# Optimization experiments

Hardware: AMD Instinct MI355X
Metric: run time of the kernel (lower is better)

The kernel has to match this reference:

```python
import jax
import jax.numpy as jnp
import numpy as np
from jax import lax

DELTA = float(np.exp(-2.0))  # rule-creation density threshold


def codebook_lamb(x):
    """Online growing RBF prototype codebook (ALMMo-style) for one layer.

    x: [N, M]. Returns lamb: [N] normalized density of each sample at its
    assigned rule. Faithful (corrected) semantics of Layer.__call__:
      - SEN = squared L2 norm per sample (over feature dim)
      - global mean / mean squared norm over the batch
      - sequential per-sample: if max RBF density over existing rules < exp(-2),
        append a new rule (prototype=c=x, SENc=||x||^2, support=1);
        else update rule_star. Note the source's `support[rule_star] = +1`
        assigns 1, so the running mean update degenerates to c[rule_star]=x,
        SENc[rule_star]=||x||^2 -- replicated here.
      - distances use the (never-updated) prototypes; bandwidth stau uses c.
    """
    N, M = x.shape
    SENx = jnp.sum(x * x, axis=-1)                      # [N]
    gmean = jnp.mean(x, axis=0)                         # [M]
    base = jnp.mean(SENx) - jnp.sum(gmean * gmean)      # SENgmean - SEN(gmean)
    R = N                                               # worst case: one rule/sample

    protos0 = jnp.zeros((R, M), x.dtype)
    pn20 = jnp.zeros((R,), x.dtype)                     # ||proto_r||^2 (carried)
    c0 = jnp.zeros((R, M), x.dtype)
    cn20 = jnp.zeros((R,), x.dtype)                     # ||c_r||^2 (carried)
    SENc0 = jnp.zeros((R,), x.dtype)
    count0 = jnp.int32(0)

    ridx = jnp.arange(R)

    def step(carry, inp):
        protos, pn2, c, cn2, SENc, count = carry
        xi, sxi = inp                                   # [M], scalar
        valid = ridx < count
        stau = (base + SENc - cn2) * 0.5                # [R]
        dist = sxi + pn2 - 2.0 * (protos @ xi)          # [R] ||xi - proto_r||^2
        dens = jnp.where(valid, jnp.exp(-dist / stau), -jnp.inf)
        idx = jnp.argmax(dens)
        vmax = dens[idx]
        new = (count == 0) | (vmax < DELTA)
        slot = jnp.where(new, count, idx)
        # both branches set c/SENc at slot to xi/sxi (support resets to 1)
        c = c.at[slot].set(xi)
        cn2 = cn2.at[slot].set(sxi)
        SENc = SENc.at[slot].set(sxi)
        # only a new rule writes a prototype (OOB scatter when count==R is dropped)
        protos = protos.at[count].set(jnp.where(new, xi, protos[count]))
        pn2 = pn2.at[count].set(jnp.where(new, sxi, pn2[count]))
        count = count + new.astype(count.dtype)
        return (protos, pn2, c, cn2, SENc, count), slot

    (protos, pn2, c, cn2, SENc, count), rules = lax.scan(
        step, (protos0, pn20, c0, cn20, SENc0, count0), (x, SENx)
    )

    # final densities of all samples under all (valid) rules: [R, N]
    stau = (base + SENc - cn2) * 0.5                    # [R]
    dist = SENx[None, :] + pn2[:, None] - 2.0 * (protos @ x.T)
    dens = jnp.where((ridx < count)[:, None], jnp.exp(-dist / stau[:, None]), 0.0)
    dens_xn = dens[rules, jnp.arange(N)]                # density at assigned rule
    lamb = dens_xn / jnp.sum(dens, axis=0)              # normalize over rules
    return lamb


def setup_inputs() -> dict:
    key = jax.random.key(0)
    k = jax.random.split(key, 5)
    N, D_IN, D_H, D_OUT = 2048, 2048, 2048, 1024
    s0 = 1.0 / np.sqrt(D_IN)
    s1 = 1.0 / np.sqrt(D_H)
    return {
        "x": jax.random.normal(k[0], (N, D_IN), jnp.float32),
        "W0": jax.random.normal(k[1], (D_H, D_IN), jnp.float32) * s0,
        "b0": jax.random.normal(k[2], (D_H,), jnp.float32) * s0,
        "W1": jax.random.normal(k[3], (D_OUT, D_H), jnp.float32) * s1,
        "b1": jax.random.normal(k[4], (D_OUT,), jnp.float32) * s1,
    }


def reference(x, W0, b0, W1, b1):
    lambs = []
    h = x
    for W, b in ((W0, b0), (W1, b1)):
        lambs.append(codebook_lamb(h))          # per-layer codebook on layer input
        h = jax.nn.sigmoid(h @ W.T + b)         # torch.nn.Linear + sigmoid
    return h, jnp.stack(lambs)                  # ([N, d_out], [n_layers, N])
```

## Files before the change

### kernel.cpp

```cpp
#include <hip/hip_runtime.h>
#include <cstdint>
#include <cstddef>


#define DELTA_F 0.13533528323661270f
#define MBYTE (1u << 20)

typedef __bf16 bf16;
typedef bf16 bf16x8 __attribute__((ext_vector_type(8)));
typedef bf16 bf16x4 __attribute__((ext_vector_type(4)));
typedef float f32x4 __attribute__((ext_vector_type(4)));

typedef __attribute__((address_space(1))) void as1_void;
typedef __attribute__((address_space(3))) void as3_void;

__device__ __forceinline__ void gload16(const bf16* g, bf16* l) {
  __builtin_amdgcn_global_load_lds((as1_void*)g, (as3_void*)l, 16, 0, 0);
}

__device__ __forceinline__ float wave_reduce(float s) {
  for (int o = 32; o > 0; o >>= 1) s += __shfl_down(s, o, 64);
  return s;
}

template <bool SAME>
__device__ void run_decide_lamb(char* smem, int* e, float* Dens, float* S,
                                float* diagD, float* lambOut) {
  char* s_flag = smem;
  short* s_as = (short*)(smem + 2048);
  short* s_list = (short*)(smem + 6144);
  short* s_re = (short*)(smem + 10240);
  int* scan_ = (int*)(smem + 14336);
  float* rbest = (float*)(smem + 16384);
  int* rbj = (int*)(smem + 18432);
  int* sT = (int*)(smem + 24576);
  int* sReN = (int*)(smem + 24580);
  const int tid = threadIdx.x;
  int cntl = 0;
#pragma unroll
  for (int k = 0; k < 4; ++k) {
    const int i = tid * 4 + k;
    const int ei = SAME ? atomicOr(e + i, 0) : e[i];
    s_flag[i] = (ei == 0);
    if (ei == 0) s_as[i] = (short)i;
    cntl += (ei != 0);
  }
  scan_[tid] = cntl;
  if (tid == 0) sReN[0] = 0;
  __syncthreads();
  for (int off = 1; off < 512; off <<= 1) {
    const int v = scan_[tid];
    const int add = (tid >= off) ? scan_[tid - off] : 0;
    __syncthreads();
    scan_[tid] = v + add;
    __syncthreads();
  }
  int pos = scan_[tid] - cntl;
#pragma unroll
  for (int k = 0; k < 4; ++k) {
    const int i = tid * 4 + k;
    if (!s_flag[i]) s_list[pos++] = (short)i;
  }
  if (tid == 511) sT[0] = scan_[511];
  __syncthreads();
  const int T = sT[0];
  if (SAME && T > 0) __threadfence();
  for (int t = 0; t < T; ++t) {
    const int i = s_list[t];
    const float* di = Dens + (size_t)i * 2048;
    float best = -1.0f;
    int bestj = 0x7fffffff;
    for (int j = tid; j < i; j += 512) {
      if (s_flag[j]) {
        const float d = di[j];
        if (d > best || (d == best && j < bestj)) { best = d; bestj = j; }
      }
    }
    rbest[tid] = best; rbj[tid] = bestj;
    __syncthreads();
    if (tid == 0) {
      float b = -1.0f;
      int bj = 0x7fffffff;
      for (int k = 0; k < 512; ++k)
        if (rbest[k] > b || (rbest[k] == b && rbj[k] < bj)) { b = rbest[k]; bj = rbj[k]; }
      if (b < DELTA_F) { s_flag[i] = 1; s_as[i] = (short)i; }
      else { s_as[i] = (short)bj; s_re[sReN[0]++] = (short)i; }
    }
    __syncthreads();
  }
  const int reN = sReN[0];
#pragma unroll
  for (int k = 0; k < 4; ++k) {
    const int n = k * 512 + tid;
    const int aa = s_as[n];
    const float num = (aa == n)
        ? (SAME ? atomicAdd(diagD + n, 0.f) : diagD[n])
        : Dens[(size_t)n * 2048 + aa];
    float denom = SAME ? atomicAdd(S + n, 0.f) : S[n];
    for (int t = 0; t < reN; ++t) denom -= Dens[(size_t)n * 2048 + s_re[t]];
    lambOut[n] = num / denom;
  }
}

template <bool IS_L0>
__global__ __launch_bounds__(512, 4) void gemm_fused(
    const bf16* __restrict__ A, float* __restrict__ Dens,
    bf16* __restrict__ Hb, float* __restrict__ Fo,
    const float* __restrict__ bias, const float* __restrict__ SENin,
    const float* __restrict__ ninv_p, float* __restrict__ S,
    int* __restrict__ e, float* __restrict__ SENhOut,
    float* __restrict__ colsumH, float* __restrict__ diagD,
    int* __restrict__ cnt, int nblocks, float* __restrict__ lambOut,
    int* __restrict__ flagN, const float* __restrict__ SENh_r,
    const float* __restrict__ colsumH_r, int* __restrict__ e0,
    float* __restrict__ S0, float* __restrict__ diag0,
    float* __restrict__ Dens0, float* __restrict__ lamb0) {
  __shared__ __align__(16) char smemA[32768];
  __shared__ __align__(16) char smemB[32768];
  __shared__ int s_last;
  const int tid = threadIdx.x;

  if (!IS_L0 && blockIdx.x == 24) {
    if (blockIdx.y != 0) return;
    float* r1 = (float*)(smemA + 20480);
    float* r2 = (float*)(smemA + 22528);
    float ssen = 0.f, sg2 = 0.f;
    for (int i = tid; i < 2048; i += 512) ssen += SENh_r[i];
    for (int c = tid; c < 2048; c += 512) {
      const float gm = colsumH_r[c] * (1.f / 2048.f);
      sg2 += gm * gm;
    }
    r1[tid] = ssen; r2[tid] = sg2;
    __syncthreads();
    for (int s = 256; s; s >>= 1) {
      if (tid < s) { r1[tid] += r1[tid + s]; r2[tid] += r2[tid + s]; }
      __syncthreads();
    }
    if (tid == 0) {
      const float stau = 0.5f * (r1[0] * (1.f / 2048.f) - r2[0]);
      atomicExch(flagN, __float_as_int(-1.f / stau));
    }
    __syncthreads();
    run_decide_lamb<false>(smemA, e0, Dens0, S0, diag0, lamb0);
    return;
  }

  const int wave = tid >> 6, lane = tid & 63;
  const int quad = lane >> 4, l16 = lane & 15;
  const int kg = wave & 1, wm = (wave >> 1) & 1, wn = (wave >> 2) & 1;
  const int m0 = blockIdx.y * 128, n0 = blockIdx.x * 128;
  const int waveM = wm * 64, waveN = wn * 64;
  const bool isGram = (n0 < 2048);
  const int sr8 = lane >> 3, slot = lane & 7;
  const int gk = (slot ^ sr8) * 8;
  const bf16* aSrc = A + (size_t)(m0 + wave * 16 + sr8) * 2048 + gk;
  const bf16* bSrc = A + (size_t)(n0 + wave * 16 + sr8) * 2048 + gk;
  char* const aDst0 = smemA + wave * 2048;
  char* const bDst0 = smemA + 16384 + wave * 2048;
  char* const aDst1 = smemB + wave * 2048;
  char* const bDst1 = smemB + 16384 + wave * 2048;
  const int swz = ((kg * 4 + quad) ^ (l16 & 7)) * 16;
  const int aOff = (waveM + l16) * 128 + swz;
  const int bOff = 16384 + (waveN + l16) * 128 + swz;

#define STAGE(aD, bD, k)                              \
  do {                                                \
    gload16(aSrc + (k), (bf16*)(aD));                 \
    gload16(aSrc + 8 * 2048 + (k), (bf16*)((aD) + 1024)); \
    gload16(bSrc + (k), (bf16*)(bD));                 \
    gload16(bSrc + 8 * 2048 + (k), (bf16*)((bD) + 1024)); \
  } while (0)

#define COMPUTE(sm)                                                        \
  do {                                                                     \
    bf16x8 af[4], bfr[4];                                                  \
    _Pragma("unroll") for (int i = 0; i < 4; ++i)                          \
        af[i] = *(const bf16x8*)((sm) + aOff + i * 2048);                  \
    _Pragma("unroll") for (int j = 0; j < 4; ++j)                          \
        bfr[j] = *(const bf16x8*)((sm) + bOff + j * 2048);                 \
    _Pragma("unroll") for (int i = 0; i < 4; ++i)                          \
        _Pragma("unroll") for (int j = 0; j < 4; ++j) acc[i][j] =          \
            __builtin_amdgcn_mfma_f32_16x16x32_bf16(af[i], bfr[j],         \
                                                    acc[i][j], 0, 0, 0);   \
  } while (0)

  f32x4 acc[4][4] = {};
  STAGE(aDst0, bDst0, 0);
  for (int k0 = 0; k0 < 2048; k0 += 128) {
    __syncthreads();
    STAGE(aDst1, bDst1, k0 + 64);
    COMPUTE(smemA);
    __syncthreads();
    if (k0 + 128 < 2048) STAGE(aDst0, bDst0, k0 + 128);
    COMPUTE(smemB);
  }
#undef STAGE
#undef COMPUTE

  float ninv = 0.f;
  if (isGram) {
    if (IS_L0) ninv = ninv_p[0];
    else {
      int fi;
      while ((fi = atomicOr(flagN, 0)) == 0) {}
      ninv = __int_as_float(fi);
    }
  }

  float colp[4] = {0.f, 0.f, 0.f, 0.f};
  char* const ex = smemA + (wn * 2 + wm) * 8192;
#pragma unroll
  for (int round = 0; round < 2; ++round) {
    __syncthreads();
    if (kg == 1) {
#pragma unroll
      for (int ii = 0; ii < 2; ++ii)
#pragma unroll
        for (int j = 0; j < 4; ++j)
          *(f32x4*)(ex + (ii * 4 + j) * 1024 + lane * 16) = acc[round * 2 + ii][j];
    }
    __syncthreads();
    if (kg == 0) {
#pragma unroll
      for (int ii = 0; ii < 2; ++ii) {
        const int i = round * 2 + ii;
        const int rbase = m0 + waveM + i * 16 + quad * 4;
        if (isGram) {
          const f32x4 si4 = *(const f32x4*)(SENin + rbase);
          float rp[4] = {0.f, 0.f, 0.f, 0.f};
          int er = 0;
#pragma unroll
          for (int j = 0; j < 4; ++j) {
            f32x4 v = acc[i][j] + *(const f32x4*)(ex + (ii * 4 + j) * 1024 + lane * 16);
            const int col = n0 + waveN + j * 16 + l16;
            const float sj = SENin[col];
#pragma unroll
            for (int r = 0; r < 4; ++r) {
              const float dens = __expf((si4[r] + sj - 2.0f * v[r]) * ninv);
              Dens[(size_t)(rbase + r) * 2048 + col] = dens;
              rp[r] += dens;
              if (col < rbase + r && dens >= DELTA_F) er |= (1 << r);
              if (col == rbase + r) atomicExch(diagD + col, dens);
            }
          }
#pragma unroll
          for (int r = 0; r < 4; ++r) {
            float rv = rp[r];
            rv += __shfl_xor(rv, 1, 64); rv += __shfl_xor(rv, 2, 64);
            rv += __shfl_xor(rv, 4, 64); rv += __shfl_xor(rv, 8, 64);
            if (l16 == 0) atomicAdd(S + rbase + r, rv);
          }
          er |= __shfl_xor(er, 1, 64); er |= __shfl_xor(er, 2, 64);
          er |= __shfl_xor(er, 4, 64); er |= __shfl_xor(er, 8, 64);
          if (l16 == 0 && er) {
#pragma unroll
            for (int r = 0; r < 4; ++r)
              if ((er >> r) & 1) atomicOr(e + rbase + r, 1);
          }
        } else {
          float rn[4] = {0.f, 0.f, 0.f, 0.f};
#pragma unroll
          for (int j = 0; j < 4; ++j) {
            f32x4 v = acc[i][j] + *(const f32x4*)(ex + (ii * 4 + j) * 1024 + lane * 16);
            const int c2 = n0 - 2048 + waveN + j * 16 + l16;
            const float bv = bias[c2];
#pragma unroll
            for (int r = 0; r < 4; ++r) {
              const float hv = 1.0f / (1.0f + __expf(-(v[r] + bv)));
              if (IS_L0) {
                Hb[(size_t)(rbase + r) * 2048 + c2] = (bf16)hv;
                rn[r] += hv * hv;
                colp[j] += hv;
              } else {
                Fo[(size_t)(rbase + r) * 1024 + c2] = hv;
              }
            }
          }
          if (IS_L0) {
#pragma unroll
            for (int r = 0; r < 4; ++r) {
              float rv = rn[r];
              rv += __shfl_xor(rv, 1, 64); rv += __shfl_xor(rv, 2, 64);
              rv += __shfl_xor(rv, 4, 64); rv += __shfl_xor(rv, 8, 64);
              if (l16 == 0) atomicAdd(SENhOut + rbase + r, rv);
            }
          }
        }
      }
    }
  }
  if (IS_L0 && !isGram && kg == 0) {
#pragma unroll
    for (int j = 0; j < 4; ++j) {
      float cv = colp[j];
      cv += __shfl_xor(cv, 16, 64);
      cv += __shfl_xor(cv, 32, 64);
      if (lane < 16) atomicAdd(colsumH + (n0 - 2048 + waveN + j * 16 + lane), cv);
    }
  }

  if (IS_L0) return;

  __syncthreads();
  if (tid == 0) s_last = (atomicAdd(cnt, 1) == nblocks - 1);
  __syncthreads();
  if (!s_last) return;
  run_decide_lamb<true>(smemA, e, Dens, S, diagD, lambOut);
}

__global__ void f2b_all(const float* __restrict__ x, const float* __restrict__ W0,
                        const float* __restrict__ W1, bf16* __restrict__ xb,
                        bf16* __restrict__ wb0, bf16* __restrict__ wb1,
                        float* __restrict__ SENx, float* __restrict__ bins,
                        int* __restrict__ cntF, float* __restrict__ scal) {
  const int b = blockIdx.x, tid = threadIdx.x;
  const int wave = tid >> 6, lane = tid & 63;
  __shared__ float ws[8][4];
  __shared__ float red1[256], red2[256];
  __shared__ int s_last;
  if (b < 256) {
    const int r0 = b * 8;
    f32x4 c0 = {0.f, 0.f, 0.f, 0.f}, c1 = {0.f, 0.f, 0.f, 0.f};
    for (int r = 0; r < 8; ++r) {
      const float* src = x + (size_t)(r0 + r) * 2048;
      bf16* dst = xb + (size_t)(r0 + r) * 2048;
      f32x4 v0 = *(const f32x4*)(src + tid * 4);
      f32x4 v1 = *(const f32x4*)(src + 1024 + tid * 4);
      bf16x4 o0, o1;
      o0.x = (bf16)v0.x; o0.y = (bf16)v0.y; o0.z = (bf16)v0.z; o0.w = (bf16)v0.w;
      o1.x = (bf16)v1.x; o1.y = (bf16)v1.y; o1.z = (bf16)v1.z; o1.w = (bf16)v1.w;
      *(bf16x4*)(dst + tid * 4) = o0;
      *(bf16x4*)(dst + 1024 + tid * 4) = o1;
      c0 += v0; c1 += v1;
      float rn = v0.x * v0.x + v0.y * v0.y + v0.z * v0.z + v0.w * v0.w +
                 v1.x * v1.x + v1.y * v1.y + v1.z * v1.z + v1.w * v1.w;
      rn = wave_reduce(rn);
      if (lane == 0) ws[r][wave] = rn;
    }
    __syncthreads();
    if (tid < 8)
      atomicExch(SENx + r0 + tid, ws[tid][0] + ws[tid][1] + ws[tid][2] + ws[tid][3]);
    float* bin = bins + (size_t)(b & 15) * 2048;
    atomicAdd(bin + tid * 4 + 0, c0.x); atomicAdd(bin + tid * 4 + 1, c0.y);
    atomicAdd(bin + tid * 4 + 2, c0.z); atomicAdd(bin + tid * 4 + 3, c0.w);
    atomicAdd(bin + 1024 + tid * 4 + 0, c1.x); atomicAdd(bin + 1024 + tid * 4 + 1, c1.y);
    atomicAdd(bin + 1024 + tid * 4 + 2, c1.z); atomicAdd(bin + 1024 + tid * 4 + 3, c1.w);
  } else if (b < 512) {
    const size_t base = (size_t)(b - 256) * 16384;
    for (int c = tid * 4; c < 16384; c += 1024) {
      f32x4 v = *(const f32x4*)(W0 + base + c);
      bf16x4 o;
      o.x = (bf16)v.x; o.y = (bf16)v.y; o.z = (bf16)v.z; o.w = (bf16)v.w;
      *(bf16x4*)(wb0 + base + c) = o;
    }
  } else {
    const size_t base = (size_t)(b - 512) * 16384;
    for (int c = tid * 4; c < 16384; c += 1024) {
      f32x4 v = *(const f32x4*)(W1 + base + c);
      bf16x4 o;
      o.x = (bf16)v.x; o.y = (bf16)v.y; o.z = (bf16)v.z; o.w = (bf16)v.w;
      *(bf16x4*)(wb1 + base + c) = o;
    }
  }

  __syncthreads();
  if (tid == 0) s_last = (atomicAdd(cntF, 1) == 639);
  __syncthreads();
  if (!s_last) return;
  float ssen = 0.f;
  for (int i = tid; i < 2048; i += 256) ssen += atomicAdd(SENx + i, 0.f);
  float sg2 = 0.f;
  for (int c = tid; c < 2048; c += 256) {
    float cs = 0.f;
#pragma unroll
    for (int p = 0; p < 16; ++p) cs += atomicAdd(bins + (size_t)p * 2048 + c, 0.f);
    const float gm = cs * (1.f / 2048.f);
    sg2 += gm * gm;
  }
  red1[tid] = ssen; red2[tid] = sg2;
  __syncthreads();
  for (int s = 128; s; s >>= 1) {
    if (tid < s) { red1[tid] += red1[tid + s]; red2[tid] += red2[tid + s]; }
    __syncthreads();
  }
  if (tid == 0) {
    const float stau = 0.5f * (red1[0] * (1.f / 2048.f) - red2[0]);
    scal[0] = stau;
    scal[1] = -1.f / stau;
  }
}

extern "C" void kernel_launch(void* const* d_in, const int* in_sizes, int n_in,
                              void* d_out, int out_size, void* d_ws, size_t ws_size,
                              hipStream_t stream) {
  const float* x = (const float*)d_in[0];
  const float* W0 = (const float*)d_in[1];
  const float* b0 = (const float*)d_in[2];
  const float* W1 = (const float*)d_in[3];
  const float* b1 = (const float*)d_in[4];
  float* out = (float*)d_out;

  char* w = (char*)d_ws;
  bf16* xb = (bf16*)(w);
  bf16* wb0 = (bf16*)(w + 8 * MBYTE);
  bf16* hb = (bf16*)(w + 16 * MBYTE);
  bf16* wb1 = (bf16*)(w + 24 * MBYTE);
  float* Dens0 = (float*)(w + 28 * MBYTE);
  float* Dens1 = (float*)(w);
  float* SENx = (float*)(w + 44 * MBYTE);
  float* scal = SENx + 2048;
  float* zre = scal + 16;
  float* bins = zre;
  float* SENh = bins + 16 * 2048;
  float* colsumH = SENh + 2048;
  float* S0 = colsumH + 2048;
  float* S1 = S0 + 2048;
  float* diagD0 = S1 + 2048;
  float* diagD1 = diagD0 + 2048;
  int* e0 = (int*)(diagD1 + 2048);
  int* e1 = e0 + 2048;
  int* cntF = e1 + 2048;
  int* cnt1 = cntF + 1;
  int* flagN = cnt1 + 1;
  const size_t zwords = 16 * 2048 + 8 * 2048 + 16;

  float* lamb0 = out + (size_t)2048 * 1024;
  float* lamb1 = lamb0 + 2048;

  hipMemsetAsync(zre, 0, zwords * 4, stream);
  f2b_all<<<640, 256, 0, stream>>>(x, W0, W1, xb, wb0, wb1, SENx, bins, cntF, scal);
  gemm_fused<true><<<dim3(32, 16), 512, 0, stream>>>(
      xb, Dens0, hb, nullptr, b0, SENx, scal + 1, S0, e0, SENh, colsumH,
      diagD0, nullptr, 0, nullptr,
      nullptr, nullptr, nullptr, nullptr, nullptr, nullptr, nullptr, nullptr);
  gemm_fused<false><<<dim3(25, 16), 512, 0, stream>>>(
      hb, Dens1, nullptr, out, b1, SENh, nullptr, S1, e1, nullptr, nullptr,
      diagD1, cnt1, 384, lamb1,
      flagN, SENh, colsumH, e0, S0, diagD0, Dens0, lamb0);
}
```

Baseline: 190.0 us.

## Use 256x128 GEMM tiles without intra-block split-K, plus XCD-aware block remap

The fused GEMM now computes 256x128 output tiles per block. Each wave owns a 64x64 sub-tile over the full K slice, replacing the old scheme where pairs of waves split K and reduced partial sums through LDS in the epilogue. Block IDs are remapped so that blocks sharing A rows land on the same XCD, which is meant to improve L2 reuse. The cost is a larger LDS footprint (96KB), launch bounds cut from 4 to 2, and half as many blocks, which lowers occupancy and may leave some CUs underfilled.

```diff
diff --git a/kernel.cpp b/kernel.cpp
--- a/kernel.cpp
+++ b/kernel.cpp
@@ -103,7 +103,7 @@
 }
 
 template <bool IS_L0>
-__global__ __launch_bounds__(512, 4) void gemm_fused(
+__global__ __launch_bounds__(512, 2) void gemm_fused(
     const bf16* __restrict__ A, float* __restrict__ Dens,
     bf16* __restrict__ Hb, float* __restrict__ Fo,
     const float* __restrict__ bias, const float* __restrict__ SENin,
@@ -115,8 +115,8 @@
     const float* __restrict__ colsumH_r, int* __restrict__ e0,
     float* __restrict__ S0, float* __restrict__ diag0,
     float* __restrict__ Dens0, float* __restrict__ lamb0) {
-  __shared__ __align__(16) char smemA[32768];
-  __shared__ __align__(16) char smemB[32768];
+  __shared__ __align__(16) char smemA[49152];
+  __shared__ __align__(16) char smemB[49152];
   __shared__ int s_last;
   const int tid = threadIdx.x;
 
@@ -145,43 +145,56 @@
     return;
   }
 
+  int bx, by;
+  if (IS_L0) {
+    const int lid = blockIdx.x + (blockIdx.y << 5);
+    by = lid & 7; bx = lid >> 3;
+  } else {
+    const int lid = blockIdx.x + blockIdx.y * 25;
+    const int xcd = lid & 7, j = lid >> 3;
+    by = xcd; bx = j - (j > 3 * (xcd + 1));
+  }
+  const int m0 = by * 256, n0 = bx * 128;
+
   const int wave = tid >> 6, lane = tid & 63;
   const int quad = lane >> 4, l16 = lane & 15;
-  const int kg = wave & 1, wm = (wave >> 1) & 1, wn = (wave >> 2) & 1;
-  const int m0 = blockIdx.y * 128, n0 = blockIdx.x * 128;
-  const int waveM = wm * 64, waveN = wn * 64;
+  const int wm = wave >> 1, wn = wave & 1;
   const bool isGram = (n0 < 2048);
   const int sr8 = lane >> 3, slot = lane & 7;
   const int gk = (slot ^ sr8) * 8;
-  const bf16* aSrc = A + (size_t)(m0 + wave * 16 + sr8) * 2048 + gk;
+  const bf16* aSrc = A + (size_t)(m0 + wave * 32 + sr8) * 2048 + gk;
   const bf16* bSrc = A + (size_t)(n0 + wave * 16 + sr8) * 2048 + gk;
-  char* const aDst0 = smemA + wave * 2048;
-  char* const bDst0 = smemA + 16384 + wave * 2048;
-  char* const aDst1 = smemB + wave * 2048;
-  char* const bDst1 = smemB + 16384 + wave * 2048;
-  const int swz = ((kg * 4 + quad) ^ (l16 & 7)) * 16;
-  const int aOff = (waveM + l16) * 128 + swz;
-  const int bOff = 16384 + (waveN + l16) * 128 + swz;
-
-#define STAGE(aD, bD, k)                              \
-  do {                                                \
-    gload16(aSrc + (k), (bf16*)(aD));                 \
-    gload16(aSrc + 8 * 2048 + (k), (bf16*)((aD) + 1024)); \
-    gload16(bSrc + (k), (bf16*)(bD));                 \
-    gload16(bSrc + 8 * 2048 + (k), (bf16*)((bD) + 1024)); \
+  char* const aDst0 = smemA + wave * 4096;
+  char* const bDst0 = smemA + 32768 + wave * 2048;
+  char* const aDst1 = smemB + wave * 4096;
+  char* const bDst1 = smemB + 32768 + wave * 2048;
+  const int aB = (wm * 64 + l16) * 128;
+  const int bB = 32768 + (wn * 64 + l16) * 128;
+
+#define STAGE(aD, bD, k)                                    \
+  do {                                                      \
+    gload16(aSrc + (k), (bf16*)(aD));                       \
+    gload16(aSrc + 8 * 2048 + (k), (bf16*)((aD) + 1024));   \
+    gload16(aSrc + 16 * 2048 + (k), (bf16*)((aD) + 2048));  \
+    gload16(aSrc + 24 * 2048 + (k), (bf16*)((aD) + 3072));  \
+    gload16(bSrc + (k), (bf16*)(bD));                       \
+    gload16(bSrc + 8 * 2048 + (k), (bf16*)((bD) + 1024));   \
   } while (0)
 
-#define COMPUTE(sm)                                                        \
-  do {                                                                     \
-    bf16x8 af[4], bfr[4];                                                  \
-    _Pragma("unroll") for (int i = 0; i < 4; ++i)                          \
-        af[i] = *(const bf16x8*)((sm) + aOff + i * 2048);                  \
-    _Pragma("unroll") for (int j = 0; j < 4; ++j)                          \
-        bfr[j] = *(const bf16x8*)((sm) + bOff + j * 2048);                 \
-    _Pragma("unroll") for (int i = 0; i < 4; ++i)                          \
-        _Pragma("unroll") for (int j = 0; j < 4; ++j) acc[i][j] =          \
-            __builtin_amdgcn_mfma_f32_16x16x32_bf16(af[i], bfr[j],         \
-                                                    acc[i][j], 0, 0, 0);   \
+#define COMPUTE(sm)                                                          \
+  do {                                                                       \
+    _Pragma("unroll") for (int ks = 0; ks < 2; ++ks) {                       \
+      bf16x8 af[4], bfr[4];                                                  \
+      const int sw = ((ks * 4 + quad) ^ (l16 & 7)) * 16;                     \
+      _Pragma("unroll") for (int i = 0; i < 4; ++i)                          \
+          af[i] = *(const bf16x8*)((sm) + aB + i * 2048 + sw);               \
+      _Pragma("unroll") for (int j = 0; j < 4; ++j)                          \
+          bfr[j] = *(const bf16x8*)((sm) + bB + j * 2048 + sw);              \
+      _Pragma("unroll") for (int i = 0; i < 4; ++i)                          \
+          _Pragma("unroll") for (int j = 0; j < 4; ++j) acc[i][j] =          \
+              __builtin_amdgcn_mfma_f32_16x16x32_bf16(af[i], bfr[j],         \
+                                                      acc[i][j], 0, 0, 0);   \
+    }                                                                        \
   } while (0)
 
   f32x4 acc[4][4] = {};
@@ -208,94 +221,78 @@
   }
 
   float colp[4] = {0.f, 0.f, 0.f, 0.f};
-  char* const ex = smemA + (wn * 2 + wm) * 8192;
-#pragma unroll
-  for (int round = 0; round < 2; ++round) {
-    __syncthreads();
-    if (kg == 1) {
-#pragma unroll
-      for (int ii = 0; ii < 2; ++ii)
-#pragma unroll
-        for (int j = 0; j < 4; ++j)
-          *(f32x4*)(ex + (ii * 4 + j) * 1024 + lane * 16) = acc[round * 2 + ii][j];
-    }
-    __syncthreads();
-    if (kg == 0) {
-#pragma unroll
-      for (int ii = 0; ii < 2; ++ii) {
-        const int i = round * 2 + ii;
-        const int rbase = m0 + waveM + i * 16 + quad * 4;
-        if (isGram) {
-          const f32x4 si4 = *(const f32x4*)(SENin + rbase);
-          float rp[4] = {0.f, 0.f, 0.f, 0.f};
-          int er = 0;
-#pragma unroll
-          for (int j = 0; j < 4; ++j) {
-            f32x4 v = acc[i][j] + *(const f32x4*)(ex + (ii * 4 + j) * 1024 + lane * 16);
-            const int col = n0 + waveN + j * 16 + l16;
-            const float sj = SENin[col];
-#pragma unroll
-            for (int r = 0; r < 4; ++r) {
-              const float dens = __expf((si4[r] + sj - 2.0f * v[r]) * ninv);
-              Dens[(size_t)(rbase + r) * 2048 + col] = dens;
-              rp[r] += dens;
-              if (col < rbase + r && dens >= DELTA_F) er |= (1 << r);
-              if (col == rbase + r) atomicExch(diagD + col, dens);
-            }
-          }
-#pragma unroll
-          for (int r = 0; r < 4; ++r) {
-            float rv = rp[r];
-            rv += __shfl_xor(rv, 1, 64); rv += __shfl_xor(rv, 2, 64);
-            rv += __shfl_xor(rv, 4, 64); rv += __shfl_xor(rv, 8, 64);
-            if (l16 == 0) atomicAdd(S + rbase + r, rv);
-          }
-          er |= __shfl_xor(er, 1, 64); er |= __shfl_xor(er, 2, 64);
-          er |= __shfl_xor(er, 4, 64); er |= __shfl_xor(er, 8, 64);
-          if (l16 == 0 && er) {
-#pragma unroll
-            for (int r = 0; r < 4; ++r)
-              if ((er >> r) & 1) atomicOr(e + rbase + r, 1);
-          }
-        } else {
-          float rn[4] = {0.f, 0.f, 0.f, 0.f};
-#pragma unroll
-          for (int j = 0; j < 4; ++j) {
-            f32x4 v = acc[i][j] + *(const f32x4*)(ex + (ii * 4 + j) * 1024 + lane * 16);
-            const int c2 = n0 - 2048 + waveN + j * 16 + l16;
-            const float bv = bias[c2];
-#pragma unroll
-            for (int r = 0; r < 4; ++r) {
-              const float hv = 1.0f / (1.0f + __expf(-(v[r] + bv)));
-              if (IS_L0) {
-                Hb[(size_t)(rbase + r) * 2048 + c2] = (bf16)hv;
-                rn[r] += hv * hv;
-                colp[j] += hv;
-              } else {
-                Fo[(size_t)(rbase + r) * 1024 + c2] = hv;
-              }
-            }
-          }
+#pragma unroll
+  for (int i = 0; i < 4; ++i) {
+    const int rbase = m0 + wm * 64 + i * 16 + quad * 4;
+    if (isGram) {
+      const f32x4 si4 = *(const f32x4*)(SENin + rbase);
+      float rp[4] = {0.f, 0.f, 0.f, 0.f};
+      int er = 0;
+#pragma unroll
+      for (int j = 0; j < 4; ++j) {
+        const f32x4 v = acc[i][j];
+        const int col = n0 + wn * 64 + j * 16 + l16;
+        const float sj = SENin[col];
+#pragma unroll
+        for (int r = 0; r < 4; ++r) {
+          const float dens = __expf((si4[r] + sj - 2.0f * v[r]) * ninv);
+          Dens[(size_t)(rbase + r) * 2048 + col] = dens;
+          rp[r] += dens;
+          if (col < rbase + r && dens >= DELTA_F) er |= (1 << r);
+          if (col == rbase + r) atomicExch(diagD + col, dens);
+        }
+      }
+#pragma unroll
+      for (int r = 0; r < 4; ++r) {
+        float rv = rp[r];
+        rv += __shfl_xor(rv, 1, 64); rv += __shfl_xor(rv, 2, 64);
+        rv += __shfl_xor(rv, 4, 64); rv += __shfl_xor(rv, 8, 64);
+        if (l16 == 0) atomicAdd(S + rbase + r, rv);
+      }
+      er |= __shfl_xor(er, 1, 64); er |= __shfl_xor(er, 2, 64);
+      er |= __shfl_xor(er, 4, 64); er |= __shfl_xor(er, 8, 64);
+      if (l16 == 0 && er) {
+#pragma unroll
+        for (int r = 0; r < 4; ++r)
+          if ((er >> r) & 1) atomicOr(e + rbase + r, 1);
+      }
+    } else {
+      float rn[4] = {0.f, 0.f, 0.f, 0.f};
+#pragma unroll
+      for (int j = 0; j < 4; ++j) {
+        const f32x4 v = acc[i][j];
+        const int c2 = n0 - 2048 + wn * 64 + j * 16 + l16;
+        const float bv = bias[c2];
+#pragma unroll
+        for (int r = 0; r < 4; ++r) {
+          const float hv = 1.0f / (1.0f + __expf(-(v[r] + bv)));
           if (IS_L0) {
-#pragma unroll
-            for (int r = 0; r < 4; ++r) {
-              float rv = rn[r];
-              rv += __shfl_xor(rv, 1, 64); rv += __shfl_xor(rv, 2, 64);
-              rv += __shfl_xor(rv, 4, 64); rv += __shfl_xor(rv, 8, 64);
-              if (l16 == 0) atomicAdd(SENhOut + rbase + r, rv);
-            }
+            Hb[(size_t)(rbase + r) * 2048 + c2] = (bf16)hv;
+            rn[r] += hv * hv;
+            colp[j] += hv;
+          } else {
+            Fo[(size_t)(rbase + r) * 1024 + c2] = hv;
           }
         }
       }
-    }
-  }
-  if (IS_L0 && !isGram && kg == 0) {
+      if (IS_L0) {
+#pragma unroll
+        for (int r = 0; r < 4; ++r) {
+          float rv = rn[r];
+          rv += __shfl_xor(rv, 1, 64); rv += __shfl_xor(rv, 2, 64);
+          rv += __shfl_xor(rv, 4, 64); rv += __shfl_xor(rv, 8, 64);
+          if (l16 == 0) atomicAdd(SENhOut + rbase + r, rv);
+        }
+      }
+    }
+  }
+  if (IS_L0 && !isGram) {
 #pragma unroll
     for (int j = 0; j < 4; ++j) {
       float cv = colp[j];
       cv += __shfl_xor(cv, 16, 64);
       cv += __shfl_xor(cv, 32, 64);
-      if (lane < 16) atomicAdd(colsumH + (n0 - 2048 + waveN + j * 16 + lane), cv);
+      if (lane < 16) atomicAdd(colsumH + (n0 - 2048 + wn * 64 + j * 16 + lane), cv);
     }
   }
 
@@ -429,12 +426,12 @@
 
   hipMemsetAsync(zre, 0, zwords * 4, stream);
   f2b_all<<<640, 256, 0, stream>>>(x, W0, W1, xb, wb0, wb1, SENx, bins, cntF, scal);
-  gemm_fused<true><<<dim3(32, 16), 512, 0, stream>>>(
+  gemm_fused<true><<<dim3(32, 8), 512, 0, stream>>>(
       xb, Dens0, hb, nullptr, b0, SENx, scal + 1, S0, e0, SENh, colsumH,
       diagD0, nullptr, 0, nullptr,
       nullptr, nullptr, nullptr, nullptr, nullptr, nullptr, nullptr, nullptr);
-  gemm_fused<false><<<dim3(25, 16), 512, 0, stream>>>(
+  gemm_fused<false><<<dim3(25, 8), 512, 0, stream>>>(
       hb, Dens1, nullptr, out, b1, SENh, nullptr, S1, e1, nullptr, nullptr,
-      diagD1, cnt1, 384, lamb1,
+      diagD1, cnt1, 192, lamb1,
       flagN, SENh, colsumH, e0, S0, diagD0, Dens0, lamb0);
 }
```

After: 196.8 us. 1.04x slower.
